# Performance work log

Hardware: AMD Instinct MI355X
Metric: run time of the kernel (lower is better)

The kernel has to match this reference:

```python
import jax, jax.numpy as jnp
import numpy as np

B, S, D, H = 4, 2048, 1024, 16
DH = D // H  # 64


def setup_inputs() -> dict:
    key = jax.random.key(0)
    ks = jax.random.split(key, 9)
    scale = 1.0 / np.sqrt(D)
    x = jax.random.normal(ks[0], (B, S, D), dtype=jnp.float32)
    # Stacked per-head projection weights, equivalent to ModuleList of Linear(D, DH)
    Wq = jax.random.uniform(ks[1], (H, D, DH), jnp.float32, -scale, scale)
    bq = jax.random.uniform(ks[2], (H, DH), jnp.float32, -scale, scale)
    Wk = jax.random.uniform(ks[3], (H, D, DH), jnp.float32, -scale, scale)
    bk = jax.random.uniform(ks[4], (H, DH), jnp.float32, -scale, scale)
    Wv = jax.random.uniform(ks[5], (H, D, DH), jnp.float32, -scale, scale)
    bv = jax.random.uniform(ks[6], (H, DH), jnp.float32, -scale, scale)
    Wo = jax.random.uniform(ks[7], (D, D), jnp.float32, -scale, scale)
    bo = jax.random.uniform(ks[8], (D,), jnp.float32, -scale, scale)
    return {"x": x, "Wq": Wq, "bq": bq, "Wk": Wk, "bk": bk,
            "Wv": Wv, "bv": bv, "Wo": Wo, "bo": bo}


def reference(x, Wq, bq, Wk, bk, Wv, bv, Wo, bo):
    # Per-head Linear projections, batched across heads: [B,S,D]x[H,D,DH] -> [B,H,S,DH]
    q = jnp.einsum('bsd,hde->bhse', x, Wq) + bq[None, :, None, :]
    k = jnp.einsum('bsd,hde->bhse', x, Wk) + bk[None, :, None, :]
    v = jnp.einsum('bsd,hde->bhse', x, Wv) + bv[None, :, None, :]
    # Scaled dot-product attention (no mask is applied in the original forward)
    scores = jnp.einsum('bhse,bhte->bhst', q, k) / jnp.sqrt(jnp.float32(DH))
    attn = jax.nn.softmax(scores, axis=-1)
    z = jnp.einsum('bhst,bhte->bhse', attn, v)  # [B,H,S,DH]
    # Concat heads on last dim (head-major order matches torch.cat over dim=-1)
    multihead = jnp.transpose(z, (0, 2, 1, 3)).reshape(B, S, D)
    return multihead @ Wo + bo
```

## Files before the change

### kernel.cpp

```cpp
#include <hip/hip_runtime.h>
#include <hip/hip_bf16.h>
#include <cstdint>
#include <cstddef>


typedef unsigned short u16;
typedef unsigned int u32;
typedef __attribute__((ext_vector_type(8))) __bf16 bf16x8;
typedef __attribute__((ext_vector_type(8))) unsigned short u16x8;
typedef __attribute__((ext_vector_type(4))) float f32x4;
typedef __attribute__((ext_vector_type(4))) unsigned int u32x4;

__device__ __forceinline__ u16 f2bf(float f) {
  union { __hip_bfloat16 h; u16 u; } c;
  c.h = __float2bfloat16(f);
  return c.u;
}
__device__ __forceinline__ u32 pk2(float a, float b) {
  return (u32)f2bf(a) | ((u32)f2bf(b) << 16);
}

__device__ __forceinline__ void async16(const void* g, void* l) {
  __builtin_amdgcn_global_load_lds(
      (const __attribute__((address_space(1))) void*)g,
      (__attribute__((address_space(3))) void*)l, 16, 0, 0);
}

__global__ void k_pack_x(const float* __restrict__ x, u16* __restrict__ xb) {
  const int i = (blockIdx.x * 256 + threadIdx.x) * 4;
  const float4 v = *(const float4*)(x + i);
  ushort4 o;
  o.x = f2bf(v.x); o.y = f2bf(v.y); o.z = f2bf(v.z); o.w = f2bf(v.w);
  *(ushort4*)(xb + i) = o;
}

__global__ void k_pack_wqkv(const float* __restrict__ Wq, const float* __restrict__ Wk,
                            const float* __restrict__ Wv, u16* __restrict__ Wt) {
  const int gid = blockIdx.x * 256 + threadIdx.x;
  const int n = gid >> 8;
  const int d0 = (gid & 255) << 2;
  const int proj = n >> 10, rem = n & 1023, h = rem >> 6, e = rem & 63;
  const float* Wp = (proj == 0) ? Wq : ((proj == 1) ? Wk : Wv);
  const float* src = Wp + h * 65536 + e;
  ushort4 o;
  o.x = f2bf(src[(d0 + 0) * 64]);
  o.y = f2bf(src[(d0 + 1) * 64]);
  o.z = f2bf(src[(d0 + 2) * 64]);
  o.w = f2bf(src[(d0 + 3) * 64]);
  *(ushort4*)(Wt + (size_t)n * 1024 + d0) = o;
}

__global__ void k_pack_bias(const float* __restrict__ bq, const float* __restrict__ bk,
                            const float* __restrict__ bv, float* __restrict__ out) {
  const int n = blockIdx.x * 256 + threadIdx.x;
  const int proj = n >> 10, rem = n & 1023, h = rem >> 6, e = rem & 63;
  const float* bp = (proj == 0) ? bq : ((proj == 1) ? bk : bv);
  out[n] = bp[h * 64 + e];
}

__global__ void k_pack_wo(const float* __restrict__ Wo, u16* __restrict__ Wot) {
  const int gid = blockIdx.x * 256 + threadIdx.x;
  const int n = gid >> 8;
  const int d0 = (gid & 255) << 2;
  ushort4 o;
  o.x = f2bf(Wo[(size_t)(d0 + 0) * 1024 + n]);
  o.y = f2bf(Wo[(size_t)(d0 + 1) * 1024 + n]);
  o.z = f2bf(Wo[(size_t)(d0 + 2) * 1024 + n]);
  o.w = f2bf(Wo[(size_t)(d0 + 3) * 1024 + n]);
  *(ushort4*)(Wot + (size_t)n * 1024 + d0) = o;
}

template <int MODE>
__global__ __launch_bounds__(256)
void k_gemm(const u16* __restrict__ A, const u16* __restrict__ Bt,
            const float* __restrict__ bias, void* __restrict__ Cout, int ldc) {
  __shared__ __align__(16) u16 Alds[128 * 32];
  __shared__ __align__(16) u16 Blds[128 * 32];
  const int t = threadIdx.x;
  const int lane = t & 63;
  const int w = t >> 6;
  const int l15 = lane & 15;
  const int quad = lane >> 4;
  const int wm = w >> 1, wn = w & 1;
  const int m0 = blockIdx.y << 7;
  const int n0 = blockIdx.x << 7;

  const u16* ga0 = A + (size_t)(m0 + (t >> 2)) * 1024 + (t & 3) * 8;
  const u16* ga1 = ga0 + (size_t)64 * 1024;
  const u16* gb0 = Bt + (size_t)(n0 + (t >> 2)) * 1024 + (t & 3) * 8;
  const u16* gb1 = gb0 + (size_t)64 * 1024;
  u16* const lA0 = Alds + w * 512;
  u16* const lA1 = Alds + w * 512 + 2048;
  u16* const lB0 = Blds + w * 512;
  u16* const lB1 = Blds + w * 512 + 2048;

  f32x4 acc[4][4];
#pragma unroll
  for (int mi = 0; mi < 4; ++mi)
#pragma unroll
    for (int ni = 0; ni < 4; ++ni) acc[mi][ni] = (f32x4){0.f, 0.f, 0.f, 0.f};

  for (int k0 = 0; k0 < 1024; k0 += 32) {
    __syncthreads();
    async16(ga0, lA0); async16(ga1, lA1);
    async16(gb0, lB0); async16(gb1, lB1);
    ga0 += 32; ga1 += 32; gb0 += 32; gb1 += 32;
    __syncthreads();
    bf16x8 af[4], bfr[4];
#pragma unroll
    for (int i = 0; i < 4; ++i) {
      af[i]  = *(const bf16x8*)(Alds + (wm * 64 + i * 16 + l15) * 32 + quad * 8);
      bfr[i] = *(const bf16x8*)(Blds + (wn * 64 + i * 16 + l15) * 32 + quad * 8);
    }
#pragma unroll
    for (int mi = 0; mi < 4; ++mi)
#pragma unroll
      for (int ni = 0; ni < 4; ++ni)
        acc[mi][ni] = __builtin_amdgcn_mfma_f32_16x16x32_bf16(af[mi], bfr[ni], acc[mi][ni], 0, 0, 0);
  }

  const int row0 = m0 + wm * 64;
  const int col0 = n0 + wn * 64;
  const float qscale = (MODE == 0 && col0 < 1024) ? 0.125f : 1.0f;
#pragma unroll
  for (int mi = 0; mi < 4; ++mi) {
#pragma unroll
    for (int ni = 0; ni < 4; ++ni) {
      const int col = col0 + ni * 16 + l15;
      const float bb = bias[col];
#pragma unroll
      for (int r = 0; r < 4; ++r) {
        const int row = row0 + mi * 16 + quad * 4 + r;
        const float v = (acc[mi][ni][r] + bb) * qscale;
        if (MODE == 0) ((u16*)Cout)[(size_t)row * ldc + col] = f2bf(v);
        else           ((float*)Cout)[(size_t)row * ldc + col] = v;
      }
    }
  }
}

__global__ __launch_bounds__(256)
void k_vt(const u16* __restrict__ qkv, u16* __restrict__ vtg) {
  __shared__ u16 tile[64][72];
  const int t = threadIdx.x;
  const int bh = blockIdx.y, b = bh >> 4, h = bh & 15;
  const int s0 = blockIdx.x << 6;
  {
    const int row = t >> 2, col0 = (t & 3) * 16;
    const u16* src = qkv + (size_t)(b * 2048 + s0 + row) * 3072 + 2048 + h * 64 + col0;
    const u16x8 v0 = *(const u16x8*)src;
    const u16x8 v1 = *(const u16x8*)(src + 8);
    *(u16x8*)&tile[row][col0] = v0;
    *(u16x8*)&tile[row][col0 + 8] = v1;
  }
  __syncthreads();
  {
    const int e = t >> 2, sc = (t & 3) * 16;
    u16 buf[16];
#pragma unroll
    for (int i = 0; i < 16; ++i) buf[i] = tile[sc + i][e];
    u16* dst = vtg + ((size_t)bh * 64 + e) * 2048 + s0 + sc;
    *(u16x8*)dst = *(const u16x8*)&buf[0];
    *(u16x8*)(dst + 8) = *(const u16x8*)&buf[8];
  }
}

__global__ __launch_bounds__(256)
void k_attn(const u16* __restrict__ qkv, const u16* __restrict__ vtg,
            u16* __restrict__ mh) {
  __shared__ __align__(16) u16 smem[16384];
  u16* const Klds = smem;
  u16* const Vlds = smem + 8192;

  const int t = threadIdx.x;
  const int lane = t & 63;
  const int w = t >> 6;
  const int l15 = lane & 15;
  const int quad = lane >> 4;
  const int bh = blockIdx.y, b = bh >> 4, h = bh & 15;
  const int s0 = blockIdx.x << 7;

  const u16* ksrc[4];
  const u16* vsrc[4];
  u16* dstK[4]; u16* dstV[4];
#pragma unroll
  for (int r = 0; r < 4; ++r) {
    const int s = t + r * 256;
    {
      const int lam = s >> 3, cs = s & 7, c = cs ^ (lam & 7);
      const int key = (lam & 0x63) | (((lam >> 2) & 3) << 3) | (((lam >> 4) & 1) << 2);
      ksrc[r] = qkv + (size_t)(b * 2048 + key) * 3072 + 1024 + h * 64 + c * 8;
    }
    {
      const int e = s >> 4, cs = s & 15, c = cs ^ (e & 15);
      vsrc[r] = vtg + ((size_t)bh * 64 + e) * 2048 + c * 8;
    }
    dstK[r] = Klds + w * 512 + r * 2048;
    dstV[r] = Vlds + w * 512 + r * 2048;
  }

#pragma unroll
  for (int r = 0; r < 4; ++r) {
    const int s = t + r * 256;
    const int lam = s >> 3, cs = s & 7, c = cs ^ (lam & 7);
    async16(qkv + (size_t)(b * 2048 + s0 + lam) * 3072 + h * 64 + c * 8, dstK[r]);
  }
  __syncthreads();
  bf16x8 aq[2][2];
#pragma unroll
  for (int g = 0; g < 2; ++g)
#pragma unroll
    for (int ks2 = 0; ks2 < 2; ++ks2) {
      const int row = w * 32 + g * 16 + l15;
      aq[g][ks2] = *(const bf16x8*)(Klds + row * 64 + ((ks2 * 4 + quad) ^ (l15 & 7)) * 8);
    }

  float lsum0 = 0.f, lsum1 = 0.f;
  f32x4 o[2][4];
#pragma unroll
  for (int g = 0; g < 2; ++g)
#pragma unroll
    for (int ne = 0; ne < 4; ++ne) o[g][ne] = (f32x4){0.f, 0.f, 0.f, 0.f};
  u32x4 pf[2][4];

  for (int kt = 0; kt < 16; ++kt) {
    __syncthreads();
#pragma unroll
    for (int r = 0; r < 4; ++r) { async16(ksrc[r], dstK[r]); ksrc[r] += 128 * 3072; }
#pragma unroll
    for (int r = 0; r < 4; ++r) { async16(vsrc[r], dstV[r]); vsrc[r] += 128; }
    __syncthreads();

#pragma unroll
    for (int kt8 = 0; kt8 < 8; ++kt8) {
      const int row = kt8 * 16 + l15;
      const bf16x8 kf0 = *(const bf16x8*)(Klds + row * 64 + ((quad) ^ (l15 & 7)) * 8);
      const bf16x8 kf1 = *(const bf16x8*)(Klds + row * 64 + ((4 + quad) ^ (l15 & 7)) * 8);
      f32x4 st0 = __builtin_amdgcn_mfma_f32_16x16x32_bf16(kf0, aq[0][0], (f32x4){0.f,0.f,0.f,0.f}, 0, 0, 0);
      st0 = __builtin_amdgcn_mfma_f32_16x16x32_bf16(kf1, aq[0][1], st0, 0, 0, 0);
      f32x4 st1 = __builtin_amdgcn_mfma_f32_16x16x32_bf16(kf0, aq[1][0], (f32x4){0.f,0.f,0.f,0.f}, 0, 0, 0);
      st1 = __builtin_amdgcn_mfma_f32_16x16x32_bf16(kf1, aq[1][1], st1, 0, 0, 0);
      const float p00 = __expf(st0[0]), p01 = __expf(st0[1]);
      const float p02 = __expf(st0[2]), p03 = __expf(st0[3]);
      const float p10 = __expf(st1[0]), p11 = __expf(st1[1]);
      const float p12 = __expf(st1[2]), p13 = __expf(st1[3]);
      lsum0 += (p00 + p01) + (p02 + p03);
      lsum1 += (p10 + p11) + (p12 + p13);
      pf[0][kt8 >> 1][(kt8 & 1) * 2 + 0] = pk2(p00, p01);
      pf[0][kt8 >> 1][(kt8 & 1) * 2 + 1] = pk2(p02, p03);
      pf[1][kt8 >> 1][(kt8 & 1) * 2 + 0] = pk2(p10, p11);
      pf[1][kt8 >> 1][(kt8 & 1) * 2 + 1] = pk2(p12, p13);
    }

#pragma unroll
    for (int ks = 0; ks < 4; ++ks) {
      const bf16x8 ap0 = __builtin_bit_cast(bf16x8, pf[0][ks]);
      const bf16x8 ap1 = __builtin_bit_cast(bf16x8, pf[1][ks]);
#pragma unroll
      for (int ne = 0; ne < 4; ++ne) {
        const int e = ne * 16 + l15;
        const bf16x8 bv8 = *(const bf16x8*)(Vlds + e * 128 + (((ks * 4 + quad) ^ l15) & 15) * 8);
        o[0][ne] = __builtin_amdgcn_mfma_f32_16x16x32_bf16(ap0, bv8, o[0][ne], 0, 0, 0);
        o[1][ne] = __builtin_amdgcn_mfma_f32_16x16x32_bf16(ap1, bv8, o[1][ne], 0, 0, 0);
      }
    }
  }

  lsum0 += __shfl_xor(lsum0, 16); lsum0 += __shfl_xor(lsum0, 32);
  lsum1 += __shfl_xor(lsum1, 16); lsum1 += __shfl_xor(lsum1, 32);
  const float inv0 = 1.f / lsum0;
  const float inv1 = 1.f / lsum1;

#pragma unroll
  for (int g = 0; g < 2; ++g) {
#pragma unroll
    for (int r = 0; r < 4; ++r) {
      const float inv = __shfl(g == 0 ? inv0 : inv1, quad * 4 + r);
      const int row = s0 + w * 32 + g * 16 + quad * 4 + r;
#pragma unroll
      for (int ne = 0; ne < 4; ++ne) {
        const int col = h * 64 + ne * 16 + l15;
        mh[(size_t)(b * 2048 + row) * 1024 + col] = f2bf(o[g][ne][r] * inv);
      }
    }
  }
}

extern "C" void kernel_launch(void* const* d_in, const int* in_sizes, int n_in,
                              void* d_out, int out_size, void* d_ws, size_t ws_size,
                              hipStream_t stream) {
  (void)in_sizes; (void)n_in; (void)out_size; (void)ws_size;
  const float* x  = (const float*)d_in[0];
  const float* Wq = (const float*)d_in[1];
  const float* bq = (const float*)d_in[2];
  const float* Wk = (const float*)d_in[3];
  const float* bk = (const float*)d_in[4];
  const float* Wv = (const float*)d_in[5];
  const float* bv = (const float*)d_in[6];
  const float* Wo = (const float*)d_in[7];
  const float* bo = (const float*)d_in[8];

  char* ws = (char*)d_ws;
  u16*   Xb   = (u16*)  (ws + 0);
  u16*   Vtg  = (u16*)  (ws + 0);
  u16*   Wt   = (u16*)  (ws + 16777216);
  float* bqkv = (float*)(ws + 23068672);
  u16*   Wot  = (u16*)  (ws + 23080960);
  u16*   QKV  = (u16*)  (ws + 25178112);
  u16*   MH   = (u16*)  (ws + 75509760);
  float* out  = (float*)d_out;

  k_pack_x   <<<8192, 256, 0, stream>>>(x, Xb);
  k_pack_wqkv<<<3072, 256, 0, stream>>>(Wq, Wk, Wv, Wt);
  k_pack_bias<<<12,   256, 0, stream>>>(bq, bk, bv, bqkv);
  k_pack_wo  <<<1024, 256, 0, stream>>>(Wo, Wot);
  k_gemm<0>  <<<dim3(24, 64), 256, 0, stream>>>(Xb, Wt, bqkv, (void*)QKV, 3072);
  k_vt       <<<dim3(32, 64), 256, 0, stream>>>(QKV, Vtg);
  k_attn     <<<dim3(16, 64), 256, 0, stream>>>(QKV, Vtg, MH);
  k_gemm<1>  <<<dim3(8, 64), 256, 0, stream>>>(MH, Wot, bo, (void*)out, 1024);
}
```

Baseline: 328.0 us.

## Double attention query tile per block, use exp2 with folded log2e, merge pack kernels

The attention kernel now handles 256 query rows per block, 64 per wave, so each K/V tile loaded into LDS feeds twice as many MFMAs. Queries are read straight from global memory into registers instead of being staged through LDS. The softmax exponent becomes a hardware exp2, with log2(e) folded into the Q scale in the QKV GEMM epilogue. The four packing kernels are merged into one launch, and k_attn gets launch_bounds(256,2). The larger per-wave register footprint (o[4][4] accumulators) and the halved grid of 512 blocks could lower occupancy or leave CUs underfilled.

```diff
diff --git a/kernel.cpp b/kernel.cpp
--- a/kernel.cpp
+++ b/kernel.cpp
@@ -19,6 +19,9 @@
 __device__ __forceinline__ u32 pk2(float a, float b) {
   return (u32)f2bf(a) | ((u32)f2bf(b) << 16);
 }
+__device__ __forceinline__ float ex2(float x) {
+  return __builtin_amdgcn_exp2f(x);
+}
 
 __device__ __forceinline__ void async16(const void* g, void* l) {
   __builtin_amdgcn_global_load_lds(
@@ -26,48 +29,50 @@
       (__attribute__((address_space(3))) void*)l, 16, 0, 0);
 }
 
-__global__ void k_pack_x(const float* __restrict__ x, u16* __restrict__ xb) {
-  const int i = (blockIdx.x * 256 + threadIdx.x) * 4;
-  const float4 v = *(const float4*)(x + i);
-  ushort4 o;
-  o.x = f2bf(v.x); o.y = f2bf(v.y); o.z = f2bf(v.z); o.w = f2bf(v.w);
-  *(ushort4*)(xb + i) = o;
-}
-
-__global__ void k_pack_wqkv(const float* __restrict__ Wq, const float* __restrict__ Wk,
-                            const float* __restrict__ Wv, u16* __restrict__ Wt) {
-  const int gid = blockIdx.x * 256 + threadIdx.x;
-  const int n = gid >> 8;
-  const int d0 = (gid & 255) << 2;
-  const int proj = n >> 10, rem = n & 1023, h = rem >> 6, e = rem & 63;
-  const float* Wp = (proj == 0) ? Wq : ((proj == 1) ? Wk : Wv);
-  const float* src = Wp + h * 65536 + e;
-  ushort4 o;
-  o.x = f2bf(src[(d0 + 0) * 64]);
-  o.y = f2bf(src[(d0 + 1) * 64]);
-  o.z = f2bf(src[(d0 + 2) * 64]);
-  o.w = f2bf(src[(d0 + 3) * 64]);
-  *(ushort4*)(Wt + (size_t)n * 1024 + d0) = o;
-}
-
-__global__ void k_pack_bias(const float* __restrict__ bq, const float* __restrict__ bk,
-                            const float* __restrict__ bv, float* __restrict__ out) {
-  const int n = blockIdx.x * 256 + threadIdx.x;
-  const int proj = n >> 10, rem = n & 1023, h = rem >> 6, e = rem & 63;
-  const float* bp = (proj == 0) ? bq : ((proj == 1) ? bk : bv);
-  out[n] = bp[h * 64 + e];
-}
-
-__global__ void k_pack_wo(const float* __restrict__ Wo, u16* __restrict__ Wot) {
-  const int gid = blockIdx.x * 256 + threadIdx.x;
-  const int n = gid >> 8;
-  const int d0 = (gid & 255) << 2;
-  ushort4 o;
-  o.x = f2bf(Wo[(size_t)(d0 + 0) * 1024 + n]);
-  o.y = f2bf(Wo[(size_t)(d0 + 1) * 1024 + n]);
-  o.z = f2bf(Wo[(size_t)(d0 + 2) * 1024 + n]);
-  o.w = f2bf(Wo[(size_t)(d0 + 3) * 1024 + n]);
-  *(ushort4*)(Wot + (size_t)n * 1024 + d0) = o;
+__global__ void k_pack_all(const float* __restrict__ x,
+                           const float* __restrict__ Wq, const float* __restrict__ Wk,
+                           const float* __restrict__ Wv,
+                           const float* __restrict__ bq, const float* __restrict__ bk,
+                           const float* __restrict__ bv,
+                           const float* __restrict__ Wo,
+                           u16* __restrict__ xb, u16* __restrict__ Wt,
+                           float* __restrict__ bqkv, u16* __restrict__ Wot) {
+  const int bid = blockIdx.x;
+  if (bid < 8192) {
+    const int i = (bid * 256 + threadIdx.x) * 4;
+    const float4 v = *(const float4*)(x + i);
+    ushort4 o;
+    o.x = f2bf(v.x); o.y = f2bf(v.y); o.z = f2bf(v.z); o.w = f2bf(v.w);
+    *(ushort4*)(xb + i) = o;
+  } else if (bid < 11264) {
+    const int gid = (bid - 8192) * 256 + threadIdx.x;
+    const int n = gid >> 8;
+    const int d0 = (gid & 255) << 2;
+    const int proj = n >> 10, rem = n & 1023, h = rem >> 6, e = rem & 63;
+    const float* Wp = (proj == 0) ? Wq : ((proj == 1) ? Wk : Wv);
+    const float* src = Wp + h * 65536 + e;
+    ushort4 o;
+    o.x = f2bf(src[(d0 + 0) * 64]);
+    o.y = f2bf(src[(d0 + 1) * 64]);
+    o.z = f2bf(src[(d0 + 2) * 64]);
+    o.w = f2bf(src[(d0 + 3) * 64]);
+    *(ushort4*)(Wt + (size_t)n * 1024 + d0) = o;
+  } else if (bid < 11276) {
+    const int n = (bid - 11264) * 256 + threadIdx.x;
+    const int proj = n >> 10, rem = n & 1023, h = rem >> 6, e = rem & 63;
+    const float* bp = (proj == 0) ? bq : ((proj == 1) ? bk : bv);
+    bqkv[n] = bp[h * 64 + e];
+  } else {
+    const int gid = (bid - 11276) * 256 + threadIdx.x;
+    const int n = gid >> 8;
+    const int d0 = (gid & 255) << 2;
+    ushort4 o;
+    o.x = f2bf(Wo[(size_t)(d0 + 0) * 1024 + n]);
+    o.y = f2bf(Wo[(size_t)(d0 + 1) * 1024 + n]);
+    o.z = f2bf(Wo[(size_t)(d0 + 2) * 1024 + n]);
+    o.w = f2bf(Wo[(size_t)(d0 + 3) * 1024 + n]);
+    *(ushort4*)(Wot + (size_t)n * 1024 + d0) = o;
+  }
 }
 
 template <int MODE>
@@ -121,7 +126,7 @@
 
   const int row0 = m0 + wm * 64;
   const int col0 = n0 + wn * 64;
-  const float qscale = (MODE == 0 && col0 < 1024) ? 0.125f : 1.0f;
+  const float qscale = (MODE == 0 && col0 < 1024) ? 0.125f * 1.4426950408889634f : 1.0f;
 #pragma unroll
   for (int mi = 0; mi < 4; ++mi) {
 #pragma unroll
@@ -165,7 +170,7 @@
   }
 }
 
-__global__ __launch_bounds__(256)
+__global__ __launch_bounds__(256, 2)
 void k_attn(const u16* __restrict__ qkv, const u16* __restrict__ vtg,
             u16* __restrict__ mh) {
   __shared__ __align__(16) u16 smem[16384];
@@ -178,7 +183,7 @@
   const int l15 = lane & 15;
   const int quad = lane >> 4;
   const int bh = blockIdx.y, b = bh >> 4, h = bh & 15;
-  const int s0 = blockIdx.x << 7;
+  const int s0 = blockIdx.x << 8;
 
   const u16* ksrc[4];
   const u16* vsrc[4];
@@ -199,29 +204,21 @@
     dstV[r] = Vlds + w * 512 + r * 2048;
   }
 
-#pragma unroll
-  for (int r = 0; r < 4; ++r) {
-    const int s = t + r * 256;
-    const int lam = s >> 3, cs = s & 7, c = cs ^ (lam & 7);
-    async16(qkv + (size_t)(b * 2048 + s0 + lam) * 3072 + h * 64 + c * 8, dstK[r]);
-  }
-  __syncthreads();
-  bf16x8 aq[2][2];
-#pragma unroll
-  for (int g = 0; g < 2; ++g)
-#pragma unroll
-    for (int ks2 = 0; ks2 < 2; ++ks2) {
-      const int row = w * 32 + g * 16 + l15;
-      aq[g][ks2] = *(const bf16x8*)(Klds + row * 64 + ((ks2 * 4 + quad) ^ (l15 & 7)) * 8);
-    }
-
-  float lsum0 = 0.f, lsum1 = 0.f;
-  f32x4 o[2][4];
-#pragma unroll
-  for (int g = 0; g < 2; ++g)
+  bf16x8 aq[4][2];
+#pragma unroll
+  for (int g = 0; g < 4; ++g)
+#pragma unroll
+    for (int ks2 = 0; ks2 < 2; ++ks2)
+      aq[g][ks2] = *(const bf16x8*)(qkv +
+          (size_t)(b * 2048 + s0 + w * 64 + g * 16 + l15) * 3072 +
+          h * 64 + ks2 * 32 + quad * 8);
+
+  float lsum[4] = {0.f, 0.f, 0.f, 0.f};
+  f32x4 o[4][4];
+#pragma unroll
+  for (int g = 0; g < 4; ++g)
 #pragma unroll
     for (int ne = 0; ne < 4; ++ne) o[g][ne] = (f32x4){0.f, 0.f, 0.f, 0.f};
-  u32x4 pf[2][4];
 
   for (int kt = 0; kt < 16; ++kt) {
     __syncthreads();
@@ -232,55 +229,59 @@
     __syncthreads();
 
 #pragma unroll
-    for (int kt8 = 0; kt8 < 8; ++kt8) {
-      const int row = kt8 * 16 + l15;
-      const bf16x8 kf0 = *(const bf16x8*)(Klds + row * 64 + ((quad) ^ (l15 & 7)) * 8);
-      const bf16x8 kf1 = *(const bf16x8*)(Klds + row * 64 + ((4 + quad) ^ (l15 & 7)) * 8);
-      f32x4 st0 = __builtin_amdgcn_mfma_f32_16x16x32_bf16(kf0, aq[0][0], (f32x4){0.f,0.f,0.f,0.f}, 0, 0, 0);
-      st0 = __builtin_amdgcn_mfma_f32_16x16x32_bf16(kf1, aq[0][1], st0, 0, 0, 0);
-      f32x4 st1 = __builtin_amdgcn_mfma_f32_16x16x32_bf16(kf0, aq[1][0], (f32x4){0.f,0.f,0.f,0.f}, 0, 0, 0);
-      st1 = __builtin_amdgcn_mfma_f32_16x16x32_bf16(kf1, aq[1][1], st1, 0, 0, 0);
-      const float p00 = __expf(st0[0]), p01 = __expf(st0[1]);
-      const float p02 = __expf(st0[2]), p03 = __expf(st0[3]);
-      const float p10 = __expf(st1[0]), p11 = __expf(st1[1]);
-      const float p12 = __expf(st1[2]), p13 = __expf(st1[3]);
-      lsum0 += (p00 + p01) + (p02 + p03);
-      lsum1 += (p10 + p11) + (p12 + p13);
-      pf[0][kt8 >> 1][(kt8 & 1) * 2 + 0] = pk2(p00, p01);
-      pf[0][kt8 >> 1][(kt8 & 1) * 2 + 1] = pk2(p02, p03);
-      pf[1][kt8 >> 1][(kt8 & 1) * 2 + 0] = pk2(p10, p11);
-      pf[1][kt8 >> 1][(kt8 & 1) * 2 + 1] = pk2(p12, p13);
-    }
-
-#pragma unroll
     for (int ks = 0; ks < 4; ++ks) {
-      const bf16x8 ap0 = __builtin_bit_cast(bf16x8, pf[0][ks]);
-      const bf16x8 ap1 = __builtin_bit_cast(bf16x8, pf[1][ks]);
+      u32x4 pf[4];
+#pragma unroll
+      for (int h2 = 0; h2 < 2; ++h2) {
+        const int kt8 = ks * 2 + h2;
+        const int row = kt8 * 16 + l15;
+        const bf16x8 kf0 = *(const bf16x8*)(Klds + row * 64 + ((quad) ^ (l15 & 7)) * 8);
+        const bf16x8 kf1 = *(const bf16x8*)(Klds + row * 64 + ((4 + quad) ^ (l15 & 7)) * 8);
+        f32x4 st[4];
+#pragma unroll
+        for (int g = 0; g < 4; ++g) {
+          st[g] = __builtin_amdgcn_mfma_f32_16x16x32_bf16(kf0, aq[g][0], (f32x4){0.f,0.f,0.f,0.f}, 0, 0, 0);
+          st[g] = __builtin_amdgcn_mfma_f32_16x16x32_bf16(kf1, aq[g][1], st[g], 0, 0, 0);
+        }
+#pragma unroll
+        for (int g = 0; g < 4; ++g) {
+          const float p0 = ex2(st[g][0]), p1 = ex2(st[g][1]);
+          const float p2 = ex2(st[g][2]), p3 = ex2(st[g][3]);
+          lsum[g] += (p0 + p1) + (p2 + p3);
+          pf[g][h2 * 2 + 0] = pk2(p0, p1);
+          pf[g][h2 * 2 + 1] = pk2(p2, p3);
+        }
+      }
 #pragma unroll
       for (int ne = 0; ne < 4; ++ne) {
         const int e = ne * 16 + l15;
         const bf16x8 bv8 = *(const bf16x8*)(Vlds + e * 128 + (((ks * 4 + quad) ^ l15) & 15) * 8);
-        o[0][ne] = __builtin_amdgcn_mfma_f32_16x16x32_bf16(ap0, bv8, o[0][ne], 0, 0, 0);
-        o[1][ne] = __builtin_amdgcn_mfma_f32_16x16x32_bf16(ap1, bv8, o[1][ne], 0, 0, 0);
+#pragma unroll
+        for (int g = 0; g < 4; ++g)
+          o[g][ne] = __builtin_amdgcn_mfma_f32_16x16x32_bf16(
+              __builtin_bit_cast(bf16x8, pf[g]), bv8, o[g][ne], 0, 0, 0);
       }
     }
   }
 
-  lsum0 += __shfl_xor(lsum0, 16); lsum0 += __shfl_xor(lsum0, 32);
-  lsum1 += __shfl_xor(lsum1, 16); lsum1 += __shfl_xor(lsum1, 32);
-  const float inv0 = 1.f / lsum0;
-  const float inv1 = 1.f / lsum1;
-
-#pragma unroll
-  for (int g = 0; g < 2; ++g) {
+  float inv[4];
+#pragma unroll
+  for (int g = 0; g < 4; ++g) {
+    lsum[g] += __shfl_xor(lsum[g], 16);
+    lsum[g] += __shfl_xor(lsum[g], 32);
+    inv[g] = 1.f / lsum[g];
+  }
+
+#pragma unroll
+  for (int g = 0; g < 4; ++g) {
 #pragma unroll
     for (int r = 0; r < 4; ++r) {
-      const float inv = __shfl(g == 0 ? inv0 : inv1, quad * 4 + r);
-      const int row = s0 + w * 32 + g * 16 + quad * 4 + r;
+      const float iv = __shfl(inv[g], quad * 4 + r);
+      const int row = s0 + w * 64 + g * 16 + quad * 4 + r;
 #pragma unroll
       for (int ne = 0; ne < 4; ++ne) {
         const int col = h * 64 + ne * 16 + l15;
-        mh[(size_t)(b * 2048 + row) * 1024 + col] = f2bf(o[g][ne][r] * inv);
+        mh[(size_t)(b * 2048 + row) * 1024 + col] = f2bf(o[g][ne][r] * iv);
       }
     }
   }
@@ -310,12 +311,10 @@
   u16*   MH   = (u16*)  (ws + 75509760);
   float* out  = (float*)d_out;
 
-  k_pack_x   <<<8192, 256, 0, stream>>>(x, Xb);
-  k_pack_wqkv<<<3072, 256, 0, stream>>>(Wq, Wk, Wv, Wt);
-  k_pack_bias<<<12,   256, 0, stream>>>(bq, bk, bv, bqkv);
-  k_pack_wo  <<<1024, 256, 0, stream>>>(Wo, Wot);
+  k_pack_all <<<12300, 256, 0, stream>>>(x, Wq, Wk, Wv, bq, bk, bv, Wo,
+                                         Xb, Wt, bqkv, Wot);
   k_gemm<0>  <<<dim3(24, 64), 256, 0, stream>>>(Xb, Wt, bqkv, (void*)QKV, 3072);
   k_vt       <<<dim3(32, 64), 256, 0, stream>>>(QKV, Vtg);
-  k_attn     <<<dim3(16, 64), 256, 0, stream>>>(QKV, Vtg, MH);
+  k_attn     <<<dim3(8, 64), 256, 0, stream>>>(QKV, Vtg, MH);
   k_gemm<1>  <<<dim3(8, 64), 256, 0, stream>>>(MH, Wot, bo, (void*)out, 1024);
 }
```

Result: slower. 372.1 us (+13.4%).
